# Optimization experiments

Measured on AMD Instinct MI355X. Metric: run time of the kernel, lower is better.

## Reference

```python
import jax, jax.numpy as jnp
import numpy as np

NEG_SLOPE = 0.2

def gat_conv(x, src, dst, W, a_src, a_dst, bias, N):
    # PyG GATConv, heads=1: h = xW; e_ij = LeakyReLU(a_src.h_j + a_dst.h_i)
    h = x @ W                                   # [N, H]
    as_ = h @ a_src                             # [N]
    ad_ = h @ a_dst                             # [N]
    e = jax.nn.leaky_relu(as_[src] + ad_[dst], NEG_SLOPE)   # [E]
    m = jax.ops.segment_max(e, dst, num_segments=N)          # per-target max
    w = jnp.exp(e - m[dst])
    denom = jax.ops.segment_sum(w, dst, num_segments=N)
    alpha = w / (denom[dst] + 1e-16)                          # [E]
    out = jax.ops.segment_sum(alpha[:, None] * h[src], dst, num_segments=N)
    return out + bias


def setup_inputs() -> dict:
    key = jax.random.key(0)
    N, E, D, H, A = 20000, 320000, 256, 256, 8
    ks = jax.random.split(key, 16)
    s = lambda k, shp, fan: jax.random.normal(k, shp, jnp.float32) * (1.0 / np.sqrt(fan))
    return {
        "obs": jax.random.normal(ks[0], (N, D), jnp.float32),
        "edge_index": jax.random.randint(ks[1], (2, E), 0, N, dtype=jnp.int32),
        "W1": s(ks[2], (D, H), D), "a1_src": s(ks[3], (H,), H), "a1_dst": s(ks[4], (H,), H), "b1": jnp.zeros((H,), jnp.float32),
        "W2": s(ks[5], (H, H), H), "a2_src": s(ks[6], (H,), H), "a2_dst": s(ks[7], (H,), H), "b2": jnp.zeros((H,), jnp.float32),
        "Wm1": s(ks[8], (H, H), H), "bm1": jnp.zeros((H,), jnp.float32),
        "Wm2": s(ks[9], (H, A), H), "bm2": jnp.zeros((A,), jnp.float32),
    }


def reference(obs, edge_index, W1, a1_src, a1_dst, b1, W2, a2_src, a2_dst, b2, Wm1, bm1, Wm2, bm2):
    N = obs.shape[0]
    loops = jnp.arange(N, dtype=edge_index.dtype)
    src = jnp.concatenate([edge_index[0], loops])   # add self-loops (PyG default)
    dst = jnp.concatenate([edge_index[1], loops])
    x = jax.nn.relu(gat_conv(obs, src, dst, W1, a1_src, a1_dst, b1, N))
    x = jax.nn.relu(gat_conv(x,   src, dst, W2, a2_src, a2_dst, b2, N))
    x = jax.nn.relu(x @ Wm1 + bm1)
    return jnp.tanh(x @ Wm2 + bm2)
```

## Files before the change

kernel.cpp:

```cpp
#include <hip/hip_runtime.h>
#include <hip/hip_bf16.h>
#include <math.h>
#include <stdio.h>

typedef __attribute__((ext_vector_type(8))) short short8;
typedef __attribute__((ext_vector_type(4))) float f32x4;
typedef __attribute__((ext_vector_type(4))) unsigned short us4;

__device__ __forceinline__ float us2f(unsigned short u) {
    return __uint_as_float(((unsigned)u) << 16);
}
__device__ __forceinline__ unsigned short f2us_rtn(float f) {
    return (unsigned short)__bfloat16_as_ushort(__float2bfloat16(f));
}

__global__ void prep_all(const float* __restrict__ Wa, const float* __restrict__ Wb,
                         const float* __restrict__ Wc,
                         unsigned short* __restrict__ HiA, unsigned short* __restrict__ LoA,
                         unsigned short* __restrict__ HiB, unsigned short* __restrict__ LoB,
                         unsigned short* __restrict__ HiC, unsigned short* __restrict__ LoC,
                         const float* __restrict__ X, unsigned short* __restrict__ Xb,
                         float* __restrict__ as1, float* __restrict__ ad1,
                         float* __restrict__ as2, float* __restrict__ ad2,
                         int* __restrict__ deg,
                         int K, int Nn, int N, int tot8) {
    const int tot = K * Nn;
    int idx = blockIdx.x * blockDim.x + threadIdx.x;
    if (idx < 3 * tot) {
        const float* W;
        unsigned short *Hi, *Lo;
        if (idx < tot) { W = Wa; Hi = HiA; Lo = LoA; }
        else if (idx < 2 * tot) { W = Wb; Hi = HiB; Lo = LoB; idx -= tot; }
        else { W = Wc; Hi = HiC; Lo = LoC; idx -= 2 * tot; }
        const int n = idx / K, k = idx - n * K;
        const float f = W[(size_t)k * Nn + n];
        const unsigned u = __float_as_uint(f);
        Hi[idx] = (unsigned short)(u >> 16);
        const float hf = __uint_as_float(u & 0xffff0000u);
        Lo[idx] = (unsigned short)(__float_as_uint(f - hf) >> 16);
        return;
    }
    idx -= 3 * tot;
    if (idx < 5 * N) {
        if (idx < N) as1[idx] = 0.f;
        else if (idx < 2 * N) ad1[idx - N] = 0.f;
        else if (idx < 3 * N) as2[idx - 2 * N] = 0.f;
        else if (idx < 4 * N) ad2[idx - 3 * N] = 0.f;
        else deg[idx - 4 * N] = 0;
        return;
    }
    idx -= 5 * N;
    if (idx < tot8) {
        const float4 a = *(const float4*)(X + (size_t)idx * 8);
        const float4 b = *(const float4*)(X + (size_t)idx * 8 + 4);
        short8 o;
        const float f[8] = {a.x, a.y, a.z, a.w, b.x, b.y, b.z, b.w};
#pragma unroll
        for (int e = 0; e < 8; e++) o[e] = (short)f2us_rtn(f[e]);
        *(short8*)(Xb + (size_t)idx * 8) = o;
    }
}

#define LP 72
template <bool BIASRELU, bool DOTS>
__global__ __launch_bounds__(256) void gemm_mfma(const unsigned short* __restrict__ A,
                                                 const unsigned short* __restrict__ Bt,
                                                 const float* __restrict__ bias,
                                                 const float* __restrict__ avs,
                                                 const float* __restrict__ avd,
                                                 float* __restrict__ as_,
                                                 float* __restrict__ ad_,
                                                 unsigned short* __restrict__ C,
                                                 int M, int Nn, int K) {
    __shared__ unsigned short sA[64 * LP];
    __shared__ unsigned short sB[128 * LP];
    const int tid = threadIdx.x;
    const int wave = tid >> 6, lane = tid & 63;
    const int m16 = lane & 15, quad = lane >> 4;
    const int row0 = blockIdx.x * 64, col0 = blockIdx.y * 128;
    const int wr = (wave >> 1) * 32, wc = (wave & 1) * 64;
    const int ar = tid >> 2, akc = (tid & 3) * 8;
    const int bkc = (tid & 7) * 8, bcb = tid >> 3;

    f32x4 acc[2][4] = {};
    for (int k0 = 0; k0 < K; k0 += 64) {
        {
            const int gr = (row0 + ar) < M ? (row0 + ar) : (M - 1);
            const unsigned short* Ap = A + (size_t)gr * K + k0 + akc;
            *(short8*)&sA[ar * LP + akc]      = *(const short8*)Ap;
            *(short8*)&sA[ar * LP + akc + 32] = *(const short8*)(Ap + 32);
        }
#pragma unroll
        for (int q = 0; q < 4; q++) {
            const int colq = bcb + 32 * q;
            *(short8*)&sB[colq * LP + bkc] =
                *(const short8*)(Bt + (size_t)(col0 + colq) * K + k0 + bkc);
        }
        __syncthreads();
#pragma unroll
        for (int ks = 0; ks < 2; ks++) {
            short8 ah[2];
#pragma unroll
            for (int mi = 0; mi < 2; mi++)
                ah[mi] = *(const short8*)&sA[(wr + mi * 16 + m16) * LP + ks * 32 + quad * 8];
#pragma unroll
            for (int ni = 0; ni < 4; ni++) {
                const short8 bv = *(const short8*)&sB[(wc + ni * 16 + m16) * LP + ks * 32 + quad * 8];
#pragma unroll
                for (int mi = 0; mi < 2; mi++)
                    acc[mi][ni] = __builtin_amdgcn_mfma_f32_16x16x32_bf16(ah[mi], bv, acc[mi][ni], 0, 0, 0);
            }
        }
        __syncthreads();
    }
    float ps[2][4] = {}, pd[2][4] = {};
#pragma unroll
    for (int mi = 0; mi < 2; mi++) {
        const int orow_base = row0 + wr + mi * 16 + quad * 4;
#pragma unroll
        for (int ni = 0; ni < 4; ni++) {
            const int ocol = col0 + wc + ni * 16 + m16;
            float asv = 0.f, adv = 0.f;
            if (DOTS) { asv = avs[ocol]; adv = avd[ocol]; }
#pragma unroll
            for (int r = 0; r < 4; r++) {
                const int orow = orow_base + r;
                if (orow < M) {
                    float v = acc[mi][ni][r];
                    if (BIASRELU) { v += bias[ocol]; v = fmaxf(v, 0.f); }
                    C[(size_t)orow * Nn + ocol] = f2us_rtn(v);
                    if (DOTS) { ps[mi][r] = fmaf(v, asv, ps[mi][r]); pd[mi][r] = fmaf(v, adv, pd[mi][r]); }
                }
            }
        }
    }
    if (DOTS) {
#pragma unroll
        for (int mi = 0; mi < 2; mi++)
#pragma unroll
            for (int r = 0; r < 4; r++) {
#pragma unroll
                for (int off = 1; off < 16; off <<= 1) {
                    ps[mi][r] += __shfl_xor(ps[mi][r], off);
                    pd[mi][r] += __shfl_xor(pd[mi][r], off);
                }
            }
        if (m16 == 0) {
#pragma unroll
            for (int mi = 0; mi < 2; mi++) {
                const int orow_base = row0 + wr + mi * 16 + quad * 4;
#pragma unroll
                for (int r = 0; r < 4; r++) {
                    const int orow = orow_base + r;
                    if (orow < M) {
                        atomicAdd(&as_[orow], ps[mi][r]);
                        atomicAdd(&ad_[orow], pd[mi][r]);
                    }
                }
            }
        }
    }
}
#undef LP

__global__ void count_kernel(const int* __restrict__ dstA, int* __restrict__ deg, int E, int Etot) {
    const int e = blockIdx.x * blockDim.x + threadIdx.x;
    if (e >= Etot) return;
    const int d = (e < E) ? dstA[e] : (e - E);
    atomicAdd(&deg[d], 1);
}

__global__ __launch_bounds__(1024) void scan_kernel(const int* __restrict__ deg,
                                                    int* __restrict__ offs,
                                                    int* __restrict__ cursor, int N) {
    __shared__ int sums[1024];
    const int t = threadIdx.x;
    const int chunk = (N + 1023) / 1024;
    const int start = t * chunk;
    int s = 0;
    for (int i = 0; i < chunk; i++) {
        const int p = start + i;
        if (p < N) s += deg[p];
    }
    sums[t] = s;
    __syncthreads();
    for (int off = 1; off < 1024; off <<= 1) {
        const int add = (t >= off) ? sums[t - off] : 0;
        __syncthreads();
        sums[t] += add;
        __syncthreads();
    }
    int run = (t > 0) ? sums[t - 1] : 0;
    for (int i = 0; i < chunk; i++) {
        const int p = start + i;
        if (p < N) { offs[p] = run; cursor[p] = run; run += deg[p]; }
    }
    if (t == 0) offs[N] = sums[1023];
}

__global__ void scatter_kernel(const int* __restrict__ srcA, const int* __restrict__ dstA,
                               int* __restrict__ cursor, int* __restrict__ esrc, int E, int Etot) {
    const int e = blockIdx.x * blockDim.x + threadIdx.x;
    if (e >= Etot) return;
    int s, d;
    if (e < E) { s = srcA[e]; d = dstA[e]; } else { s = d = e - E; }
    const int slot = atomicAdd(&cursor[d], 1);
    esrc[slot] = s;
}

__global__ __launch_bounds__(128) void agg_kernel(const unsigned short* __restrict__ hb,
                                                  const int* __restrict__ offs,
                                                  const int* __restrict__ esrc,
                                                  const float* __restrict__ as_,
                                                  const float* __restrict__ ad_,
                                                  const float* __restrict__ bias,
                                                  unsigned short* __restrict__ xout, int N) {
    const int n = blockIdx.x;
    const int f0 = threadIdx.x * 2;
    const int b = offs[n], e2 = offs[n + 1];
    const float adn = ad_[n];
    float ax = 0.f, ay = 0.f, wsum = 0.f;
    int j = b;
    for (; j + 8 <= e2; j += 8) {
        int s[8];
#pragma unroll
        for (int u = 0; u < 8; u++) s[u] = esrc[j + u];
        unsigned pv[8];
#pragma unroll
        for (int u = 0; u < 8; u++) pv[u] = *(const unsigned*)(hb + (size_t)s[u] * 256 + f0);
        float w[8];
#pragma unroll
        for (int u = 0; u < 8; u++) {
            float v = as_[s[u]] + adn;
            v = v > 0.f ? v : 0.2f * v;
            w[u] = __expf(v);
        }
#pragma unroll
        for (int u = 0; u < 8; u++) {
            ax = fmaf(w[u], us2f((unsigned short)(pv[u] & 0xffffu)), ax);
            ay = fmaf(w[u], us2f((unsigned short)(pv[u] >> 16)), ay);
            wsum += w[u];
        }
    }
    for (; j < e2; j++) {
        const int s = esrc[j];
        float v = as_[s] + adn;
        v = v > 0.f ? v : 0.2f * v;
        const float w = __expf(v);
        const unsigned pv = *(const unsigned*)(hb + (size_t)s * 256 + f0);
        ax = fmaf(w, us2f((unsigned short)(pv & 0xffffu)), ax);
        ay = fmaf(w, us2f((unsigned short)(pv >> 16)), ay);
        wsum += w;
    }
    const float inv = 1.0f / (wsum + 1e-16f);
    float rx = ax * inv + bias[f0];
    float ry = ay * inv + bias[f0 + 1];
    rx = rx > 0.f ? rx : 0.f;
    ry = ry > 0.f ? ry : 0.f;
    const unsigned pack = (unsigned)f2us_rtn(rx) | ((unsigned)f2us_rtn(ry) << 16);
    *(unsigned*)(xout + (size_t)n * 256 + f0) = pack;
}

__global__ __launch_bounds__(256) void final_kernel(const unsigned short* __restrict__ xb,
                                                    const float* __restrict__ W,
                                                    const float* __restrict__ bias,
                                                    float* __restrict__ out, int N, int A) {
    const int wave = threadIdx.x >> 6, lane = threadIdx.x & 63;
    const int n = blockIdx.x * 4 + wave;
    if (n >= N) return;
    const int k0 = lane * 4;
    const us4 v = *(const us4*)(xb + (size_t)n * 256 + k0);
    float p[8] = {};
#pragma unroll
    for (int e = 0; e < 4; e++) {
        const float xv = us2f(v[e]);
#pragma unroll
        for (int a = 0; a < 8; a++) p[a] = fmaf(xv, W[(k0 + e) * A + a], p[a]);
    }
#pragma unroll
    for (int off = 32; off; off >>= 1)
#pragma unroll
        for (int a = 0; a < 8; a++) p[a] += __shfl_down(p[a], off);
    if (lane == 0) {
        for (int a = 0; a < A; a++) out[(size_t)n * A + a] = tanhf(p[a] + bias[a]);
    }
}

__global__ void guard_kernel(const float* __restrict__ out) {
    if (threadIdx.x != 0 || blockIdx.x != 0) return;
    const float o0 = out[0];
    if (fabsf(o0) > 0.f && o0 == o0) return;
    printf("GUARD o0=%e o1=%e\n", (double)o0, (double)out[1]);
}

extern "C" void kernel_launch(void* const* d_in, const int* in_sizes, int n_in,
                              void* d_out, int out_size, void* d_ws, size_t ws_size,
                              hipStream_t stream) {
    const float* obs = (const float*)d_in[0];
    const int* eidx  = (const int*)d_in[1];
    const float* W1  = (const float*)d_in[2];
    const float* a1s = (const float*)d_in[3];
    const float* a1d = (const float*)d_in[4];
    const float* b1  = (const float*)d_in[5];
    const float* W2  = (const float*)d_in[6];
    const float* a2s = (const float*)d_in[7];
    const float* a2d = (const float*)d_in[8];
    const float* b2v = (const float*)d_in[9];
    const float* Wm1 = (const float*)d_in[10];
    const float* bm1 = (const float*)d_in[11];
    const float* Wm2 = (const float*)d_in[12];
    const float* bm2 = (const float*)d_in[13];
    float* out = (float*)d_out;

    const int Hh = in_sizes[3];
    const int Dd = in_sizes[2] / Hh;
    const int N  = in_sizes[0] / Dd;
    const int E  = in_sizes[1] / 2;
    const int Etot = E + N;
    const int Aout = in_sizes[12] / Hh;

    const int* srcA = eidx;
    const int* dstA = eidx + E;

    size_t off = 0;
    char* ws = (char*)d_ws;
    auto alloc = [&](size_t bytes) -> char* {
        char* p = ws + off;
        off = (off + bytes + 15) & ~(size_t)15;
        return p;
    };
    unsigned short* obs_b = (unsigned short*)alloc((size_t)N * Dd * 2);
    unsigned short* h     = (unsigned short*)alloc((size_t)N * Hh * 2);
    unsigned short* xb    = (unsigned short*)alloc((size_t)N * Hh * 2);
    float* as1   = (float*)alloc((size_t)N * 4);
    float* ad1   = (float*)alloc((size_t)N * 4);
    float* as2   = (float*)alloc((size_t)N * 4);
    float* ad2   = (float*)alloc((size_t)N * 4);
    int* deg     = (int*)alloc((size_t)N * 4);
    int* offs    = (int*)alloc((size_t)(N + 1) * 4);
    int* cursor  = (int*)alloc((size_t)N * 4);
    int* esrc    = (int*)alloc((size_t)Etot * 4);
    const size_t wsz = (size_t)Dd * Hh;
    unsigned short* W1tH = (unsigned short*)alloc(wsz * 2);
    unsigned short* W1tL = (unsigned short*)alloc(wsz * 2);
    unsigned short* W2tH = (unsigned short*)alloc(wsz * 2);
    unsigned short* W2tL = (unsigned short*)alloc(wsz * 2);
    unsigned short* WmtH = (unsigned short*)alloc(wsz * 2);
    unsigned short* WmtL = (unsigned short*)alloc(wsz * 2);

    const int eb = 256;
    const int eg = (Etot + eb - 1) / eb;
    const dim3 ggrid((N + 63) / 64, Hh / 128);
    const int nb4 = (N + 3) / 4;

    const int tot8 = (N * Dd) / 8;
    const int ptot = 3 * (int)wsz + 5 * N + tot8;
    prep_all<<<(ptot + 255) / 256, 256, 0, stream>>>(
        W1, W2, Wm1, W1tH, W1tL, W2tH, W2tL, WmtH, WmtL,
        obs, obs_b, as1, ad1, as2, ad2, deg, Dd, Hh, N, tot8);

    count_kernel<<<eg, eb, 0, stream>>>(dstA, deg, E, Etot);
    scan_kernel<<<1, 1024, 0, stream>>>(deg, offs, cursor, N);
    scatter_kernel<<<eg, eb, 0, stream>>>(srcA, dstA, cursor, esrc, E, Etot);

    gemm_mfma<false, true><<<ggrid, 256, 0, stream>>>(obs_b, W1tH, nullptr, a1s, a1d,
                                                      as1, ad1, h, N, Hh, Dd);
    agg_kernel<<<N, 128, 0, stream>>>(h, offs, esrc, as1, ad1, b1, xb, N);

    gemm_mfma<false, true><<<ggrid, 256, 0, stream>>>(xb, W2tH, nullptr, a2s, a2d,
                                                      as2, ad2, h, N, Hh, Hh);
    agg_kernel<<<N, 128, 0, stream>>>(h, offs, esrc, as2, ad2, b2v, xb, N);

    gemm_mfma<true, false><<<ggrid, 256, 0, stream>>>(xb, WmtH, bm1, nullptr, nullptr,
                                                      nullptr, nullptr, h, N, Hh, Hh);
    final_kernel<<<nb4, 256, 0, stream>>>(h, Wm2, bm2, out, N, Aout);

    guard_kernel<<<1, 64, 0, stream>>>(out);
}
```

Measured before the change: 284.6 us.

## Fuse MLP head into one GEMM kernel, widen aggregation, drop guard and hi/lo weights

Several changes land together. The third GEMM and the final 256x8 projection plus tanh are fused into a new gemm_head kernel that keeps the hidden activations in registers and LDS instead of writing them to global memory. The aggregation kernel now processes one node per wave with 4 features per lane instead of one node per 128-thread block. Weight prep writes a single round-to-nearest bf16 copy rather than hi/lo split copies, and the debug guard kernel is removed. Together these cut launches and memory traffic, at the cost of a heavier register footprint in the fused head kernel.

```diff
diff --git a/kernel.cpp b/kernel.cpp
--- a/kernel.cpp
+++ b/kernel.cpp
@@ -16,9 +16,8 @@
 
 __global__ void prep_all(const float* __restrict__ Wa, const float* __restrict__ Wb,
                          const float* __restrict__ Wc,
-                         unsigned short* __restrict__ HiA, unsigned short* __restrict__ LoA,
-                         unsigned short* __restrict__ HiB, unsigned short* __restrict__ LoB,
-                         unsigned short* __restrict__ HiC, unsigned short* __restrict__ LoC,
+                         unsigned short* __restrict__ TA, unsigned short* __restrict__ TB,
+                         unsigned short* __restrict__ TC,
                          const float* __restrict__ X, unsigned short* __restrict__ Xb,
                          float* __restrict__ as1, float* __restrict__ ad1,
                          float* __restrict__ as2, float* __restrict__ ad2,
@@ -28,16 +27,12 @@
     int idx = blockIdx.x * blockDim.x + threadIdx.x;
     if (idx < 3 * tot) {
         const float* W;
-        unsigned short *Hi, *Lo;
-        if (idx < tot) { W = Wa; Hi = HiA; Lo = LoA; }
-        else if (idx < 2 * tot) { W = Wb; Hi = HiB; Lo = LoB; idx -= tot; }
-        else { W = Wc; Hi = HiC; Lo = LoC; idx -= 2 * tot; }
+        unsigned short* T;
+        if (idx < tot) { W = Wa; T = TA; }
+        else if (idx < 2 * tot) { W = Wb; T = TB; idx -= tot; }
+        else { W = Wc; T = TC; idx -= 2 * tot; }
         const int n = idx / K, k = idx - n * K;
-        const float f = W[(size_t)k * Nn + n];
-        const unsigned u = __float_as_uint(f);
-        Hi[idx] = (unsigned short)(u >> 16);
-        const float hf = __uint_as_float(u & 0xffff0000u);
-        Lo[idx] = (unsigned short)(__float_as_uint(f - hf) >> 16);
+        T[idx] = f2us_rtn(W[(size_t)k * Nn + n]);
         return;
     }
     idx -= 3 * tot;
@@ -62,10 +57,8 @@
 }
 
 #define LP 72
-template <bool BIASRELU, bool DOTS>
 __global__ __launch_bounds__(256) void gemm_mfma(const unsigned short* __restrict__ A,
                                                  const unsigned short* __restrict__ Bt,
-                                                 const float* __restrict__ bias,
                                                  const float* __restrict__ avs,
                                                  const float* __restrict__ avd,
                                                  float* __restrict__ as_,
@@ -120,45 +113,138 @@
 #pragma unroll
         for (int ni = 0; ni < 4; ni++) {
             const int ocol = col0 + wc + ni * 16 + m16;
-            float asv = 0.f, adv = 0.f;
-            if (DOTS) { asv = avs[ocol]; adv = avd[ocol]; }
+            const float asv = avs[ocol], adv = avd[ocol];
 #pragma unroll
             for (int r = 0; r < 4; r++) {
                 const int orow = orow_base + r;
                 if (orow < M) {
-                    float v = acc[mi][ni][r];
-                    if (BIASRELU) { v += bias[ocol]; v = fmaxf(v, 0.f); }
+                    const float v = acc[mi][ni][r];
                     C[(size_t)orow * Nn + ocol] = f2us_rtn(v);
-                    if (DOTS) { ps[mi][r] = fmaf(v, asv, ps[mi][r]); pd[mi][r] = fmaf(v, adv, pd[mi][r]); }
+                    ps[mi][r] = fmaf(v, asv, ps[mi][r]);
+                    pd[mi][r] = fmaf(v, adv, pd[mi][r]);
                 }
             }
         }
     }
-    if (DOTS) {
+#pragma unroll
+    for (int mi = 0; mi < 2; mi++)
+#pragma unroll
+        for (int r = 0; r < 4; r++)
+#pragma unroll
+            for (int off = 1; off < 16; off <<= 1) {
+                ps[mi][r] += __shfl_xor(ps[mi][r], off);
+                pd[mi][r] += __shfl_xor(pd[mi][r], off);
+            }
+    if (m16 == 0) {
+#pragma unroll
+        for (int mi = 0; mi < 2; mi++) {
+            const int orow_base = row0 + wr + mi * 16 + quad * 4;
+#pragma unroll
+            for (int r = 0; r < 4; r++) {
+                const int orow = orow_base + r;
+                if (orow < M) {
+                    atomicAdd(&as_[orow], ps[mi][r]);
+                    atomicAdd(&ad_[orow], pd[mi][r]);
+                }
+            }
+        }
+    }
+}
+
+__global__ __launch_bounds__(256) void gemm_head(const unsigned short* __restrict__ A,
+                                                 const unsigned short* __restrict__ Bt,
+                                                 const float* __restrict__ bias1,
+                                                 const float* __restrict__ W2,
+                                                 const float* __restrict__ bias2,
+                                                 float* __restrict__ out,
+                                                 int M, int K, int Aout) {
+    __shared__ unsigned short sA[64 * LP];
+    __shared__ unsigned short sB[256 * LP];
+    __shared__ float pLDS[2][64][8];
+    const int tid = threadIdx.x;
+    const int wave = tid >> 6, lane = tid & 63;
+    const int m16 = lane & 15, quad = lane >> 4;
+    const int row0 = blockIdx.x * 64;
+    const int wr = (wave >> 1) * 32, wc = (wave & 1) * 128;
+    const int ar = tid >> 2, akc = (tid & 3) * 8;
+    const int bkc = (tid & 7) * 8, bcb = tid >> 3;
+
+    f32x4 acc[2][8] = {};
+    for (int k0 = 0; k0 < K; k0 += 64) {
+        {
+            const int gr = (row0 + ar) < M ? (row0 + ar) : (M - 1);
+            const unsigned short* Ap = A + (size_t)gr * K + k0 + akc;
+            *(short8*)&sA[ar * LP + akc]      = *(const short8*)Ap;
+            *(short8*)&sA[ar * LP + akc + 32] = *(const short8*)(Ap + 32);
+        }
+#pragma unroll
+        for (int q = 0; q < 8; q++) {
+            const int colq = bcb + 32 * q;
+            *(short8*)&sB[colq * LP + bkc] =
+                *(const short8*)(Bt + (size_t)colq * K + k0 + bkc);
+        }
+        __syncthreads();
+#pragma unroll
+        for (int ks = 0; ks < 2; ks++) {
+            short8 ah[2];
+#pragma unroll
+            for (int mi = 0; mi < 2; mi++)
+                ah[mi] = *(const short8*)&sA[(wr + mi * 16 + m16) * LP + ks * 32 + quad * 8];
+#pragma unroll
+            for (int ni = 0; ni < 8; ni++) {
+                const short8 bv = *(const short8*)&sB[(wc + ni * 16 + m16) * LP + ks * 32 + quad * 8];
+#pragma unroll
+                for (int mi = 0; mi < 2; mi++)
+                    acc[mi][ni] = __builtin_amdgcn_mfma_f32_16x16x32_bf16(ah[mi], bv, acc[mi][ni], 0, 0, 0);
+            }
+        }
+        __syncthreads();
+    }
+    float p[2][4][8] = {};
+#pragma unroll
+    for (int ni = 0; ni < 8; ni++) {
+        const int ocol = wc + ni * 16 + m16;
+        const float b1v = bias1[ocol];
+        float w2[8];
+#pragma unroll
+        for (int a = 0; a < 8; a++) w2[a] = W2[ocol * 8 + a];
 #pragma unroll
         for (int mi = 0; mi < 2; mi++)
 #pragma unroll
             for (int r = 0; r < 4; r++) {
-#pragma unroll
-                for (int off = 1; off < 16; off <<= 1) {
-                    ps[mi][r] += __shfl_xor(ps[mi][r], off);
-                    pd[mi][r] += __shfl_xor(pd[mi][r], off);
-                }
-            }
-        if (m16 == 0) {
-#pragma unroll
-            for (int mi = 0; mi < 2; mi++) {
-                const int orow_base = row0 + wr + mi * 16 + quad * 4;
-#pragma unroll
-                for (int r = 0; r < 4; r++) {
-                    const int orow = orow_base + r;
-                    if (orow < M) {
-                        atomicAdd(&as_[orow], ps[mi][r]);
-                        atomicAdd(&ad_[orow], pd[mi][r]);
-                    }
-                }
-            }
-        }
+                const float v = fmaxf(acc[mi][ni][r] + b1v, 0.f);
+#pragma unroll
+                for (int a = 0; a < 8; a++) p[mi][r][a] = fmaf(v, w2[a], p[mi][r][a]);
+            }
+    }
+#pragma unroll
+    for (int off = 1; off < 16; off <<= 1)
+#pragma unroll
+        for (int mi = 0; mi < 2; mi++)
+#pragma unroll
+            for (int r = 0; r < 4; r++)
+#pragma unroll
+                for (int a = 0; a < 8; a++) p[mi][r][a] += __shfl_xor(p[mi][r][a], off);
+    if (m16 == 0) {
+        const int half = wc >> 7;
+#pragma unroll
+        for (int mi = 0; mi < 2; mi++) {
+            const int lrow = wr + mi * 16 + quad * 4;
+#pragma unroll
+            for (int r = 0; r < 4; r++)
+#pragma unroll
+                for (int a = 0; a < 8; a++) pLDS[half][lrow + r][a] = p[mi][r][a];
+        }
+    }
+    __syncthreads();
+#pragma unroll
+    for (int u = 0; u < 2; u++) {
+        const int idx = tid * 2 + u;
+        const int lrow = idx >> 3, a = idx & 7;
+        const int orow = row0 + lrow;
+        if (orow < M && a < Aout)
+            out[(size_t)orow * Aout + a] =
+                tanhf(pLDS[0][lrow][a] + pLDS[1][lrow][a] + bias2[a]);
     }
 }
 #undef LP
@@ -208,26 +294,28 @@
     esrc[slot] = s;
 }
 
-__global__ __launch_bounds__(128) void agg_kernel(const unsigned short* __restrict__ hb,
+__global__ __launch_bounds__(256) void agg_kernel(const unsigned short* __restrict__ hb,
                                                   const int* __restrict__ offs,
                                                   const int* __restrict__ esrc,
                                                   const float* __restrict__ as_,
                                                   const float* __restrict__ ad_,
                                                   const float* __restrict__ bias,
                                                   unsigned short* __restrict__ xout, int N) {
-    const int n = blockIdx.x;
-    const int f0 = threadIdx.x * 2;
+    const int n = blockIdx.x * 4 + (threadIdx.x >> 6);
+    if (n >= N) return;
+    const int lane = threadIdx.x & 63;
+    const int f0 = lane * 4;
     const int b = offs[n], e2 = offs[n + 1];
     const float adn = ad_[n];
-    float ax = 0.f, ay = 0.f, wsum = 0.f;
+    float a0 = 0.f, a1 = 0.f, a2 = 0.f, a3 = 0.f, wsum = 0.f;
     int j = b;
     for (; j + 8 <= e2; j += 8) {
         int s[8];
 #pragma unroll
         for (int u = 0; u < 8; u++) s[u] = esrc[j + u];
-        unsigned pv[8];
-#pragma unroll
-        for (int u = 0; u < 8; u++) pv[u] = *(const unsigned*)(hb + (size_t)s[u] * 256 + f0);
+        us4 pv[8];
+#pragma unroll
+        for (int u = 0; u < 8; u++) pv[u] = *(const us4*)(hb + (size_t)s[u] * 256 + f0);
         float w[8];
 #pragma unroll
         for (int u = 0; u < 8; u++) {
@@ -237,8 +325,10 @@
         }
 #pragma unroll
         for (int u = 0; u < 8; u++) {
-            ax = fmaf(w[u], us2f((unsigned short)(pv[u] & 0xffffu)), ax);
-            ay = fmaf(w[u], us2f((unsigned short)(pv[u] >> 16)), ay);
+            a0 = fmaf(w[u], us2f(pv[u][0]), a0);
+            a1 = fmaf(w[u], us2f(pv[u][1]), a1);
+            a2 = fmaf(w[u], us2f(pv[u][2]), a2);
+            a3 = fmaf(w[u], us2f(pv[u][3]), a3);
             wsum += w[u];
         }
     }
@@ -247,50 +337,21 @@
         float v = as_[s] + adn;
         v = v > 0.f ? v : 0.2f * v;
         const float w = __expf(v);
-        const unsigned pv = *(const unsigned*)(hb + (size_t)s * 256 + f0);
-        ax = fmaf(w, us2f((unsigned short)(pv & 0xffffu)), ax);
-        ay = fmaf(w, us2f((unsigned short)(pv >> 16)), ay);
+        const us4 pv = *(const us4*)(hb + (size_t)s * 256 + f0);
+        a0 = fmaf(w, us2f(pv[0]), a0);
+        a1 = fmaf(w, us2f(pv[1]), a1);
+        a2 = fmaf(w, us2f(pv[2]), a2);
+        a3 = fmaf(w, us2f(pv[3]), a3);
         wsum += w;
     }
     const float inv = 1.0f / (wsum + 1e-16f);
-    float rx = ax * inv + bias[f0];
-    float ry = ay * inv + bias[f0 + 1];
-    rx = rx > 0.f ? rx : 0.f;
-    ry = ry > 0.f ? ry : 0.f;
-    const unsigned pack = (unsigned)f2us_rtn(rx) | ((unsigned)f2us_rtn(ry) << 16);
-    *(unsigned*)(xout + (size_t)n * 256 + f0) = pack;
-}
-
-__global__ __launch_bounds__(256) void final_kernel(const unsigned short* __restrict__ xb,
-                                                    const float* __restrict__ W,
-                                                    const float* __restrict__ bias,
-                                                    float* __restrict__ out, int N, int A) {
-    const int wave = threadIdx.x >> 6, lane = threadIdx.x & 63;
-    const int n = blockIdx.x * 4 + wave;
-    if (n >= N) return;
-    const int k0 = lane * 4;
-    const us4 v = *(const us4*)(xb + (size_t)n * 256 + k0);
-    float p[8] = {};
-#pragma unroll
-    for (int e = 0; e < 4; e++) {
-        const float xv = us2f(v[e]);
-#pragma unroll
-        for (int a = 0; a < 8; a++) p[a] = fmaf(xv, W[(k0 + e) * A + a], p[a]);
-    }
-#pragma unroll
-    for (int off = 32; off; off >>= 1)
-#pragma unroll
-        for (int a = 0; a < 8; a++) p[a] += __shfl_down(p[a], off);
-    if (lane == 0) {
-        for (int a = 0; a < A; a++) out[(size_t)n * A + a] = tanhf(p[a] + bias[a]);
-    }
-}
-
-__global__ void guard_kernel(const float* __restrict__ out) {
-    if (threadIdx.x != 0 || blockIdx.x != 0) return;
-    const float o0 = out[0];
-    if (fabsf(o0) > 0.f && o0 == o0) return;
-    printf("GUARD o0=%e o1=%e\n", (double)o0, (double)out[1]);
+    float r0 = fmaxf(a0 * inv + bias[f0], 0.f);
+    float r1 = fmaxf(a1 * inv + bias[f0 + 1], 0.f);
+    float r2 = fmaxf(a2 * inv + bias[f0 + 2], 0.f);
+    float r3 = fmaxf(a3 * inv + bias[f0 + 3], 0.f);
+    us4 o;
+    o[0] = f2us_rtn(r0); o[1] = f2us_rtn(r1); o[2] = f2us_rtn(r2); o[3] = f2us_rtn(r3);
+    *(us4*)(xout + (size_t)n * 256 + f0) = o;
 }
 
 extern "C" void kernel_launch(void* const* d_in, const int* in_sizes, int n_in,
@@ -341,39 +402,29 @@
     int* cursor  = (int*)alloc((size_t)N * 4);
     int* esrc    = (int*)alloc((size_t)Etot * 4);
     const size_t wsz = (size_t)Dd * Hh;
-    unsigned short* W1tH = (unsigned short*)alloc(wsz * 2);
-    unsigned short* W1tL = (unsigned short*)alloc(wsz * 2);
-    unsigned short* W2tH = (unsigned short*)alloc(wsz * 2);
-    unsigned short* W2tL = (unsigned short*)alloc(wsz * 2);
-    unsigned short* WmtH = (unsigned short*)alloc(wsz * 2);
-    unsigned short* WmtL = (unsigned short*)alloc(wsz * 2);
+    unsigned short* W1t = (unsigned short*)alloc(wsz * 2);
+    unsigned short* W2t = (unsigned short*)alloc(wsz * 2);
+    unsigned short* Wmt = (unsigned short*)alloc(wsz * 2);
 
     const int eb = 256;
     const int eg = (Etot + eb - 1) / eb;
     const dim3 ggrid((N + 63) / 64, Hh / 128);
-    const int nb4 = (N + 3) / 4;
+    const int nrow = (N + 63) / 64;
 
     const int tot8 = (N * Dd) / 8;
     const int ptot = 3 * (int)wsz + 5 * N + tot8;
     prep_all<<<(ptot + 255) / 256, 256, 0, stream>>>(
-        W1, W2, Wm1, W1tH, W1tL, W2tH, W2tL, WmtH, WmtL,
-        obs, obs_b, as1, ad1, as2, ad2, deg, Dd, Hh, N, tot8);
+        W1, W2, Wm1, W1t, W2t, Wmt, obs, obs_b, as1, ad1, as2, ad2, deg, Dd, Hh, N, tot8);
 
     count_kernel<<<eg, eb, 0, stream>>>(dstA, deg, E, Etot);
     scan_kernel<<<1, 1024, 0, stream>>>(deg, offs, cursor, N);
     scatter_kernel<<<eg, eb, 0, stream>>>(srcA, dstA, cursor, esrc, E, Etot);
 
-    gemm_mfma<false, true><<<ggrid, 256, 0, stream>>>(obs_b, W1tH, nullptr, a1s, a1d,
-                                                      as1, ad1, h, N, Hh, Dd);
-    agg_kernel<<<N, 128, 0, stream>>>(h, offs, esrc, as1, ad1, b1, xb, N);
-
-    gemm_mfma<false, true><<<ggrid, 256, 0, stream>>>(xb, W2tH, nullptr, a2s, a2d,
-                                                      as2, ad2, h, N, Hh, Hh);
-    agg_kernel<<<N, 128, 0, stream>>>(h, offs, esrc, as2, ad2, b2v, xb, N);
-
-    gemm_mfma<true, false><<<ggrid, 256, 0, stream>>>(xb, WmtH, bm1, nullptr, nullptr,
-                                                      nullptr, nullptr, h, N, Hh, Hh);
-    final_kernel<<<nb4, 256, 0, stream>>>(h, Wm2, bm2, out, N, Aout);
-
-    guard_kernel<<<1, 64, 0, stream>>>(out);
-}
+    gemm_mfma<<<ggrid, 256, 0, stream>>>(obs_b, W1t, a1s, a1d, as1, ad1, h, N, Hh, Dd);
+    agg_kernel<<<(N + 3) / 4, 256, 0, stream>>>(h, offs, esrc, as1, ad1, b1, xb, N);
+
+    gemm_mfma<<<ggrid, 256, 0, stream>>>(xb, W2t, a2s, a2d, as2, ad2, h, N, Hh, Hh);
+    agg_kernel<<<(N + 3) / 4, 256, 0, stream>>>(h, offs, esrc, as2, ad2, b2v, xb, N);
+
+    gemm_head<<<nrow, 256, 0, stream>>>(xb, Wmt, bm1, Wm2, bm2, out, N, Hh, Aout);
+}
```

Result: faster. 266.0 us (-6.6%).
